# Kernel optimization log

Hardware: AMD Instinct MI355X
Metric: run time of the kernel (lower is better)

The kernel has to match this reference:

```python
import jax, jax.numpy as jnp
import numpy as np

N = 120000   # current nodes
F = 256      # num_feat
H = 256      # num_hidden
L = 64       # num_logits
E_MP = 1000000  # message-passing edges
E = 200000      # scored edges
PREV = [60000, 80000, 100000]
PROX_WEIGHT = 0.3


def setup_inputs() -> dict:
    key = jax.random.key(0)
    ks = jax.random.split(key, 40)
    n = lambda k, shape, s=0.05: jax.random.normal(k, shape, dtype=jnp.float32) * s
    inp = {}
    inp["x"] = n(ks[0], (N, F), 1.0)
    inp["mp_adj"] = jax.random.randint(ks[1], (2, E_MP), 0, N)
    inp["edges"] = jax.random.randint(ks[2], (2, E), 0, N)
    inp["index"] = jax.random.randint(ks[3], (E,), 0, E)
    inp["prev_emb0"] = n(ks[4], (PREV[0], H), 1.0)
    inp["prev_emb1"] = n(ks[5], (PREV[1], H), 1.0)
    inp["prev_emb2"] = n(ks[6], (PREV[2], H), 1.0)
    # Module_L params
    inp["gc1_W"] = n(ks[7], (F, H))
    inp["gc1_b"] = jnp.zeros((H,), jnp.float32)
    inp["gc2_W"] = n(ks[8], (H, H))
    inp["gc2_b"] = jnp.zeros((H,), jnp.float32)
    inp["linear_W"] = n(ks[9], (2 * H, H))
    inp["linear_b"] = jnp.zeros((H,), jnp.float32)
    inp["weight_lin"] = n(ks[10], (H, H))
    inp["bias_lin"] = jnp.zeros((H,), jnp.float32)
    inp["w_q"] = n(ks[11], (H, H))
    inp["w_k"] = n(ks[12], (H, H))
    inp["w_v"] = n(ks[13], (H, H))
    # ensemble params
    inp["ml_w1"] = n(ks[14], (2 * H, H)); inp["ml_b1"] = jnp.zeros((H,), jnp.float32)
    inp["ml_w2"] = n(ks[15], (H, 1));     inp["ml_b2"] = jnp.zeros((1,), jnp.float32)
    inp["ms_w1"] = n(ks[16], (2 * H, H)); inp["ms_b1"] = jnp.zeros((H,), jnp.float32)
    inp["ms_w2"] = n(ks[17], (H, 1));     inp["ms_b2"] = jnp.zeros((1,), jnp.float32)
    inp["msdr_w"] = n(ks[18], (L, H));    inp["msdr_b"] = jnp.zeros((H,), jnp.float32)
    # Module_S logits and precomputed score tables
    inp["logits"] = n(ks[19], (N, L), 1.0)
    inp["ms_train_score"] = jax.random.uniform(ks[20], (E,), dtype=jnp.float32)
    inp["prox_train_score"] = jax.random.uniform(ks[21], (E,), dtype=jnp.float32)
    return inp


def _gcn(x, W, b, src, dst, n_nodes):
    xw = x @ W
    loop = jnp.arange(n_nodes)
    s = jnp.concatenate([src, loop])
    d = jnp.concatenate([dst, loop])
    deg = jax.ops.segment_sum(jnp.ones_like(d, dtype=xw.dtype), d, num_segments=n_nodes)
    dinv = jax.lax.rsqrt(jnp.maximum(deg, 1.0))
    norm = (dinv[s] * dinv[d])[:, None]
    out = jax.ops.segment_sum(xw[s] * norm, d, num_segments=n_nodes)
    return out + b


def _mean_max(a, b):
    return jnp.concatenate([(a + b) * 0.5, jnp.maximum(a, b)], axis=1)


def reference(x, mp_adj, edges, index, prev_emb0, prev_emb1, prev_emb2,
              gc1_W, gc1_b, gc2_W, gc2_b, linear_W, linear_b,
              weight_lin, bias_lin, w_q, w_k, w_v,
              ml_w1, ml_b1, ml_w2, ml_b2, ms_w1, ms_b1, ms_w2, ms_b2,
              msdr_w, msdr_b, logits, ms_train_score, prox_train_score):
    src_mp, dst_mp = mp_adj[0], mp_adj[1]
    # --- Module_L: 2-layer GCN encoder (dropout = identity in eval) ---
    h = jnp.tanh(_gcn(x, gc1_W, gc1_b, src_mp, dst_mp, N))
    emb = jnp.tanh(_gcn(h, gc2_W, gc2_b, src_mp, dst_mp, N))

    # --- ragged per-window temporal attention over previous snapshots ---
    prev = [prev_emb0, prev_emb1, prev_emb2]
    T = len(prev)
    start = 0
    parts = []
    for i in range(T):
        end = prev[i].shape[0]
        if end == N:
            break
        # stack snapshots i..T-1 plus current, restricted to window [start:end)
        stack = jnp.stack([prev[j][start:end] for j in range(i, T)] + [emb[start:end]], axis=0)  # [S,n,H]
        q = emb[start:end] @ w_q              # [n,H]
        k = stack @ w_k                        # [S,n,H]
        v = stack @ w_v                        # [S,n,H]
        attn = jnp.einsum('nh,snh->ns', q, k) / np.sqrt(np.float32(H))
        w = jax.nn.softmax(attn, axis=-1)      # [n,S]
        parts.append(jnp.einsum('ns,snh->nh', w, v))
        start = end
    if start != N:
        parts.append(emb[start:] @ w_v)
    attn_emb = jnp.concatenate(parts, axis=0)  # [N,H]

    emb2 = jnp.tanh(jnp.concatenate([emb, attn_emb], axis=1) @ linear_W + linear_b)  # [N,H]

    # --- symmetric bilinear edge scores ---
    sym = (weight_lin + weight_lin.T) * 0.5
    es, ed = edges[0], edges[1]
    sim = ((emb2[es] @ sym) * emb2[ed] + bias_lin).sum(axis=1)
    ml_scores = jax.nn.sigmoid(sim)            # [E]

    # --- Module_S / Proximity: table lookups ---
    ms_scores = ms_train_score[index]
    prox_scores = prox_train_score[index]

    # --- ensemble weighted sum ---
    scores = jnp.stack([ml_scores, ms_scores, prox_scores], axis=1)  # [E,3]
    ml_feat = _mean_max(emb2[es], emb2[ed])                          # [E,2H]
    a_ml = jnp.tanh(jnp.tanh(ml_feat @ ml_w1 + ml_b1) @ ml_w2 + ml_b2)
    r0 = jnp.tanh(logits[es] @ msdr_w + msdr_b)
    r1 = jnp.tanh(logits[ed] @ msdr_w + msdr_b)
    a_ms = jnp.tanh(jnp.tanh(_mean_max(r0, r1) @ ms_w1 + ms_b1) @ ms_w2 + ms_b2)
    a_px = jnp.full_like(a_ml, PROX_WEIGHT)
    attn_w = jax.nn.softmax(jnp.concatenate([a_ml, a_ms, a_px], axis=1), axis=1)  # [E,3]
    final = jnp.clip((scores * attn_w).sum(axis=1), 0.0, 1.0)
    return final
```

## Files before the change

### kernel.cpp

```cpp
#include <hip/hip_runtime.h>
#include <hip/hip_bf16.h>

#define Nn_   120000
#define F_    256
#define H_    256
#define L_    64
#define EMP_  1000000
#define E_    200000
#define P0_   60000
#define P1_   80000
#define P2_   100000
#define PROXW 0.3f

typedef __attribute__((ext_vector_type(8))) short bf16x8;
typedef __attribute__((ext_vector_type(4))) float f32x4;

__device__ inline float bf2f(unsigned short u) {
    union { unsigned int i; float f; } x; x.i = ((unsigned int)u) << 16; return x.f;
}
__device__ inline unsigned short f2bf(float f) {
    union { float f; unsigned int i; } x; x.f = f;
    unsigned int r = x.i + 0x7fffu + ((x.i >> 16) & 1u);
    return (unsigned short)(r >> 16);
}
__device__ inline float tanh_fast(float x) {
    float e = __expf(2.0f * x);
    return 1.0f - 2.0f * __builtin_amdgcn_rcpf(e + 1.0f);
}
__device__ inline float sigmoid_fast(float z) {
    return __builtin_amdgcn_rcpf(1.0f + __expf(-z));
}
__device__ inline int lds_off(int row, int s) {
    return row * 64 + ((s ^ ((row >> 1) & 3)) << 4);
}
__device__ inline void gload_lds16(const void* g, void* l) {
    __builtin_amdgcn_global_load_lds((const __attribute__((address_space(1))) void*)g,
                                     (__attribute__((address_space(3))) void*)l, 16, 0, 0);
}
__device__ inline void unpk8(uint4 u, float* o) {
    o[0] = bf2f(u.x & 0xffff); o[1] = bf2f(u.x >> 16);
    o[2] = bf2f(u.y & 0xffff); o[3] = bf2f(u.y >> 16);
    o[4] = bf2f(u.z & 0xffff); o[5] = bf2f(u.z >> 16);
    o[6] = bf2f(u.w & 0xffff); o[7] = bf2f(u.w >> 16);
}
__device__ inline void meanmax_u(unsigned int ua, unsigned int ub,
                                 unsigned int& um, unsigned int& ux) {
    float alo = __uint_as_float(ua << 16);
    float ahi = __uint_as_float(ua & 0xffff0000u);
    float blo = __uint_as_float(ub << 16);
    float bhi = __uint_as_float(ub & 0xffff0000u);
    um = (unsigned int)f2bf((alo + blo) * 0.5f) |
         ((unsigned int)f2bf((ahi + bhi) * 0.5f) << 16);
    ux = (__float_as_uint(fmaxf(alo, blo)) >> 16) |
         (__float_as_uint(fmaxf(ahi, bhi)) & 0xffff0000u);
}
__device__ inline float dot2_u(unsigned int ug, unsigned int ub) {
    float gl = __uint_as_float(ug << 16);
    float gh = __uint_as_float(ug & 0xffff0000u);
    float bl = __uint_as_float(ub << 16);
    float bh = __uint_as_float(ub & 0xffff0000u);
    return fmaf(gl, bl, gh * bh);
}

__global__ void k_count(const int* __restrict__ dst, int* __restrict__ cnt, int n) {
    int e = blockIdx.x * 256 + threadIdx.x;
    if (e < n) atomicAdd(&cnt[dst[e]], 1);
}
__global__ void k_block_reduce(const int* __restrict__ cnt, int* __restrict__ bsum, int n) {
    __shared__ int s[256];
    int i = blockIdx.x * 256 + threadIdx.x;
    s[threadIdx.x] = (i < n) ? cnt[i] : 0;
    __syncthreads();
    for (int o = 128; o > 0; o >>= 1) {
        if (threadIdx.x < o) s[threadIdx.x] += s[threadIdx.x + o];
        __syncthreads();
    }
    if (threadIdx.x == 0) bsum[blockIdx.x] = s[0];
}
__global__ void k_scan_bsum(int* bsum, int nb) {
    if (threadIdx.x == 0 && blockIdx.x == 0) {
        int acc = 0;
        for (int i = 0; i < nb; i++) { int v = bsum[i]; bsum[i] = acc; acc += v; }
    }
}
__global__ void k_scan_final(const int* __restrict__ cnt, const int* __restrict__ bsum,
                             int* __restrict__ rowp, int n, int etot) {
    __shared__ int s[256];
    int tid = threadIdx.x;
    int i = blockIdx.x * 256 + tid;
    int v = (i < n) ? cnt[i] : 0;
    s[tid] = v;
    __syncthreads();
    for (int o = 1; o < 256; o <<= 1) {
        int t = 0;
        if (tid >= o) t = s[tid - o];
        __syncthreads();
        s[tid] += t;
        __syncthreads();
    }
    if (i < n) rowp[i] = bsum[blockIdx.x] + s[tid] - v;
    if (i == 0 && blockIdx.x == 0) rowp[n] = etot;
}
__global__ void k_fill(const int* __restrict__ src, const int* __restrict__ dst,
                       const int* __restrict__ rowp, int* __restrict__ fill,
                       int* __restrict__ csr, int n) {
    int e = blockIdx.x * 256 + threadIdx.x;
    if (e < n) {
        int d = dst[e];
        int p = atomicAdd(&fill[d], 1);
        csr[rowp[d] + p] = src[e];
    }
}
__global__ void k_dinv(const int* __restrict__ cnt, float* __restrict__ dinv, int n) {
    int i = blockIdx.x * 256 + threadIdx.x;
    if (i < n) dinv[i] = rsqrtf((float)cnt[i] + 1.0f);
}

#define TM 64
#define TN 64
#define TK 16
template <bool TRANSB>
__global__ void gemm_tiled(const float* __restrict__ A, const float* __restrict__ B,
                           float* __restrict__ C, int M, int K, int N) {
    __shared__ float As[TK][TM + 4];
    __shared__ float Bs[TK][TN + 4];
    int tid = threadIdx.x;
    int tx = tid & 15, ty = tid >> 4;
    int row0 = blockIdx.y * TM, col0 = blockIdx.x * TN;
    int lr = tid >> 2, lc4 = (tid & 3) * 4;
    float acc[4][4] = {};
    for (int k0 = 0; k0 < K; k0 += TK) {
        {
            int gr = row0 + lr;
            float4 v = make_float4(0.f, 0.f, 0.f, 0.f);
            if (gr < M) v = *(const float4*)(A + (size_t)gr * K + k0 + lc4);
            As[lc4 + 0][lr] = v.x; As[lc4 + 1][lr] = v.y;
            As[lc4 + 2][lr] = v.z; As[lc4 + 3][lr] = v.w;
        }
        {
            int n = tid & 63, kk0 = tid >> 6;
#pragma unroll
            for (int p = 0; p < 4; p++) {
                int kk = kk0 + p * 4;
                if (TRANSB) Bs[kk][n] = B[(size_t)(col0 + n) * K + k0 + kk];
                else        Bs[kk][n] = B[(size_t)(k0 + kk) * N + col0 + n];
            }
        }
        __syncthreads();
#pragma unroll
        for (int kk = 0; kk < TK; kk++) {
            float4 a = *(const float4*)&As[kk][ty * 4];
            float4 b = *(const float4*)&Bs[kk][tx * 4];
            float av[4] = {a.x, a.y, a.z, a.w};
            float bv[4] = {b.x, b.y, b.z, b.w};
#pragma unroll
            for (int i = 0; i < 4; i++)
#pragma unroll
                for (int j = 0; j < 4; j++) acc[i][j] += av[i] * bv[j];
        }
        __syncthreads();
    }
#pragma unroll
    for (int i = 0; i < 4; i++) {
        int r = row0 + ty * 4 + i;
        if (r >= M) continue;
#pragma unroll
        for (int j = 0; j < 4; j++) C[(size_t)r * N + col0 + tx * 4 + j] = acc[i][j];
    }
}

__global__ void k_cvt(const float* __restrict__ in, unsigned short* __restrict__ out, int n4) {
    int i = blockIdx.x * 256 + threadIdx.x;
    if (i >= n4) return;
    float4 v = ((const float4*)in)[i];
    ushort4 o;
    o.x = f2bf(v.x); o.y = f2bf(v.y); o.z = f2bf(v.z); o.w = f2bf(v.w);
    ((ushort4*)out)[i] = o;
}

__device__ inline void packBF_task(const float* __restrict__ Wsrc,
                                   unsigned short* __restrict__ P, int blk) {
    int t = blk * 256 + threadIdx.x;
    int c = t >> 6, l = t & 63;
    int os = c >> 5, half = (c >> 4) & 1, colb = c & 15;
    int col = (colb << 4) + (l & 15);
    int k = (half << 8) + (os << 5) + ((l >> 4) << 3);
    bf16x8 v;
#pragma unroll
    for (int j = 0; j < 8; ++j) v[j] = (short)f2bf(Wsrc[(size_t)(k + j) * 256 + col]);
    *(bf16x8*)(P + (size_t)t * 8) = v;
}

__global__ void k_prep1(const float* __restrict__ gc1W, const float* __restrict__ gc2W,
                        const float* __restrict__ msdrW, const float* __restrict__ wlin,
                        const float* __restrict__ blin, const float* __restrict__ mlw1,
                        const float* __restrict__ msw1,
                        unsigned short* __restrict__ gc1Wt, unsigned short* __restrict__ gc2Wt,
                        unsigned short* __restrict__ msdrWt, unsigned short* __restrict__ symb,
                        float* __restrict__ sumb, unsigned short* __restrict__ mlPk,
                        unsigned short* __restrict__ msPk) {
    __shared__ float s[256];
    int b = blockIdx.x, tid = threadIdx.x;
    if (b < 256) {
        int c = b;
        for (int r = tid; r < 256; r += 256) gc1Wt[c * 256 + r] = f2bf(gc1W[(size_t)r * 256 + c]);
    } else if (b < 512) {
        int c = b - 256;
        for (int r = tid; r < 256; r += 256) gc2Wt[c * 256 + r] = f2bf(gc2W[(size_t)r * 256 + c]);
    } else if (b < 768) {
        int c = b - 512;
        if (tid < 64) msdrWt[c * 64 + tid] = f2bf(msdrW[(size_t)tid * 256 + c]);
    } else if (b < 1024) {
        int r = b - 768, c = tid;
        symb[r * 256 + c] = f2bf(0.5f * (wlin[r * 256 + c] + wlin[c * 256 + r]));
    } else if (b == 1024) {
        s[tid] = blin[tid];
        __syncthreads();
        for (int o = 128; o > 0; o >>= 1) {
            if (tid < o) s[tid] += s[tid + o];
            __syncthreads();
        }
        if (tid == 0) sumb[0] = s[0];
    } else if (b < 1089) {
        packBF_task(mlw1, mlPk, b - 1025);
    } else {
        packBF_task(msw1, msPk, b - 1089);
    }
}
__global__ void k_prep2(const float* __restrict__ Mqk, const float* __restrict__ linW,
                        const float* __restrict__ W2w, unsigned short* __restrict__ MqkT,
                        unsigned short* __restrict__ Bt) {
    int b = blockIdx.x, tid = threadIdx.x;
    if (b < 256) {
        int c = b;
        for (int r = tid; r < 256; r += 256) MqkT[c * 256 + r] = f2bf(Mqk[(size_t)r * 256 + c]);
    } else {
        int idx = (b - 256) * 256 + tid;
        int n = idx >> 9, k = idx & 511;
        float v = (k < 256) ? linW[(size_t)k * 256 + n] : W2w[(size_t)(k - 256) * 256 + n];
        Bt[idx] = f2bf(v);
    }
}

__global__ __launch_bounds__(256)
void k_agg_bf(const unsigned short* __restrict__ xw, const int* __restrict__ rowp,
              const int* __restrict__ csr, const float* __restrict__ dinv,
              const float* __restrict__ bias, unsigned short* __restrict__ out) {
    int w = threadIdx.x >> 6, lane = threadIdx.x & 63;
    int v = blockIdx.x * 4 + w;
    if (v >= Nn_) return;
    const uint2* x64 = (const uint2*)xw;
    uint2 us = x64[(size_t)v * 64 + lane];
    float dv = dinv[v];
    float4 bv = *(const float4*)(bias + lane * 4);
    float a0 = 0.f, a1 = 0.f, a2 = 0.f, a3 = 0.f;
    int beg = rowp[v], end = rowp[v + 1];
    uint2 u0 = make_uint2(0, 0), u1 = make_uint2(0, 0);
    uint2 u2 = make_uint2(0, 0), u3 = make_uint2(0, 0);
    float e0 = 0.f, e1 = 0.f, e2 = 0.f, e3 = 0.f;
    if (beg < end)     { int s = csr[beg];     e0 = dinv[s]; u0 = x64[(size_t)s * 64 + lane]; }
    if (beg + 1 < end) { int s = csr[beg + 1]; e1 = dinv[s]; u1 = x64[(size_t)s * 64 + lane]; }
    if (beg + 2 < end) { int s = csr[beg + 2]; e2 = dinv[s]; u2 = x64[(size_t)s * 64 + lane]; }
    if (beg + 3 < end) { int s = csr[beg + 3]; e3 = dinv[s]; u3 = x64[(size_t)s * 64 + lane]; }
    #pragma unroll 4
    for (int p = beg; p < end; ++p) {
        uint2 uc = u0; float dc = e0;
        u0 = u1; e0 = e1;
        u1 = u2; e1 = e2;
        u2 = u3; e2 = e3;
        if (p + 4 < end) {
            int s = csr[p + 4];
            e3 = dinv[s];
            u3 = x64[(size_t)s * 64 + lane];
        }
        a0 += bf2f(uc.x & 0xffff) * dc;
        a1 += bf2f(uc.x >> 16) * dc;
        a2 += bf2f(uc.y & 0xffff) * dc;
        a3 += bf2f(uc.y >> 16) * dc;
    }
    a0 = a0 * dv + bf2f(us.x & 0xffff) * dv * dv;
    a1 = a1 * dv + bf2f(us.x >> 16) * dv * dv;
    a2 = a2 * dv + bf2f(us.y & 0xffff) * dv * dv;
    a3 = a3 * dv + bf2f(us.y >> 16) * dv * dv;
    uint2 ov;
    ov.x = (unsigned int)f2bf(tanh_fast(a0 + bv.x)) |
           ((unsigned int)f2bf(tanh_fast(a1 + bv.y)) << 16);
    ov.y = (unsigned int)f2bf(tanh_fast(a2 + bv.z)) |
           ((unsigned int)f2bf(tanh_fast(a3 + bv.w)) << 16);
    ((uint2*)out)[(size_t)v * 64 + lane] = ov;
}

template <bool BIAS, bool TANH>
__global__ __launch_bounds__(256)
void mfma_gemm(const unsigned short* __restrict__ A0, const unsigned short* __restrict__ A1,
               int Ksplit, int K, const unsigned short* __restrict__ Bt,
               const float* __restrict__ bias, unsigned short* __restrict__ Cb, int M) {
    __shared__ char lds[2][16384];
    int tid = threadIdx.x, lane = tid & 63, w = tid >> 6;
    int row0 = blockIdx.y * 128, col0 = blockIdx.x * 128;
    int wr = w >> 1, wc = w & 1;
    f32x4 acc[4][4] = {};
    int nk = K >> 5;

    auto stage = [&](int ks, int buf) {
        int k0 = ks << 5;
        #pragma unroll
        for (int j = 0; j < 4; ++j) {
            int ins = w + (j << 2);
            int lrow = ((ins & 7) << 4) + (lane >> 2);
            int p = lane & 3;
            int slog = p ^ ((lrow >> 1) & 3);
            char* ldst = lds[buf] + ((ins & 7) << 10) + ((ins >= 8) ? 8192 : 0);
            const unsigned short* src;
            if (ins < 8) {
                int grow = row0 + lrow;
                if (grow >= M) grow = M - 1;
                const unsigned short* Asrc; int kk, pitch;
                if (k0 < Ksplit) { Asrc = A0; kk = k0; pitch = Ksplit; }
                else             { Asrc = A1; kk = k0 - Ksplit; pitch = K - Ksplit; }
                src = Asrc + (size_t)grow * pitch + kk + (slog << 3);
            } else {
                int grow = col0 + lrow;
                src = Bt + (size_t)grow * K + k0 + (slog << 3);
            }
            gload_lds16(src, ldst);
        }
    };

    stage(0, 0);
    for (int ks = 0; ks < nk; ++ks) {
        int cur = ks & 1;
        if (ks + 1 < nk) {
            stage(ks + 1, cur ^ 1);
            asm volatile("s_waitcnt vmcnt(4)" ::: "memory");
        } else {
            asm volatile("s_waitcnt vmcnt(0)" ::: "memory");
        }
        __builtin_amdgcn_s_barrier();
        __builtin_amdgcn_sched_barrier(0);
        int s = lane >> 4, r16 = lane & 15;
        bf16x8 a[4], b[4];
        #pragma unroll
        for (int m = 0; m < 4; ++m) a[m] = *(const bf16x8*)(lds[cur] + lds_off(wr * 64 + m * 16 + r16, s));
        #pragma unroll
        for (int n = 0; n < 4; ++n) b[n] = *(const bf16x8*)(lds[cur] + 8192 + lds_off(wc * 64 + n * 16 + r16, s));
        __builtin_amdgcn_s_setprio(1);
        #pragma unroll
        for (int m = 0; m < 4; ++m)
            #pragma unroll
            for (int n = 0; n < 4; ++n)
                acc[m][n] = __builtin_amdgcn_mfma_f32_16x16x32_bf16(a[m], b[n], acc[m][n], 0, 0, 0);
        __builtin_amdgcn_s_setprio(0);
        __builtin_amdgcn_s_barrier();
        __builtin_amdgcn_sched_barrier(0);
    }
    int q = lane >> 4, r16 = lane & 15;
    float bv[4];
    #pragma unroll
    for (int n = 0; n < 4; ++n) bv[n] = BIAS ? bias[col0 + wc * 64 + n * 16 + r16] : 0.f;
    #pragma unroll
    for (int m = 0; m < 4; ++m) {
        #pragma unroll
        for (int i = 0; i < 4; ++i) {
            int row = row0 + wr * 64 + m * 16 + q * 4 + i;
            if (row >= M) continue;
            #pragma unroll
            for (int n = 0; n < 4; ++n) {
                int col = col0 + wc * 64 + n * 16 + r16;
                float v = acc[m][n][i];
                if (BIAS) v += bv[n];
                if (TANH) v = tanh_fast(v);
                Cb[(size_t)row * 256 + col] = f2bf(v);
            }
        }
    }
}

__global__ __launch_bounds__(256)
void k_attn_u2(const unsigned short* __restrict__ emb, const unsigned short* __restrict__ t,
               const float* __restrict__ p0, const float* __restrict__ p1,
               const float* __restrict__ p2, unsigned short* __restrict__ u) {
    int tid = threadIdx.x;
    int g = tid >> 4, l = tid & 15;
    int n = blockIdx.x * 16 + g;
    size_t eoff = (size_t)n * 256 + l * 16;
    const uint4* e16 = (const uint4*)(emb + eoff);
    uint4* u16 = (uint4*)(u + eoff);
    uint4 eb0 = e16[0], eb1 = e16[1];
    if (n >= P2_) { u16[0] = eb0; u16[1] = eb1; return; }
    float tv[16], ev[16];
    {
        const uint4* t16 = (const uint4*)(t + eoff);
        unpk8(t16[0], tv); unpk8(t16[1], tv + 8);
        unpk8(eb0, ev); unpk8(eb1, ev + 8);
    }
    float m = -3.0e38f, den = 0.f, o[16];
    #pragma unroll
    for (int i = 0; i < 16; i++) o[i] = 0.f;
    auto accum = [&](const float* sv) {
        float dt = 0.f;
        #pragma unroll
        for (int i = 0; i < 16; i++) dt += tv[i] * sv[i];
        dt += __shfl_xor(dt, 1);
        dt += __shfl_xor(dt, 2);
        dt += __shfl_xor(dt, 4);
        dt += __shfl_xor(dt, 8);
        float lg = dt * 0.0625f;
        float mn = fmaxf(m, lg);
        float s0 = __expf(m - mn), s1 = __expf(lg - mn);
        den = den * s0 + s1;
        #pragma unroll
        for (int i = 0; i < 16; i++) o[i] = o[i] * s0 + s1 * sv[i];
        m = mn;
    };
    auto accum_f32 = [&](const float* base) {
        float sv[16];
        const float4* b4 = (const float4*)(base + eoff);
        #pragma unroll
        for (int i = 0; i < 4; i++) {
            float4 q = b4[i];
            sv[4 * i] = q.x; sv[4 * i + 1] = q.y; sv[4 * i + 2] = q.z; sv[4 * i + 3] = q.w;
        }
        accum(sv);
    };
    if (n < P0_)      { accum_f32(p0); accum_f32(p1); accum_f32(p2); }
    else if (n < P1_) { accum_f32(p1); accum_f32(p2); }
    else              { accum_f32(p2); }
    accum(ev);
    float inv = __builtin_amdgcn_rcpf(den);
    unsigned short h[16];
    #pragma unroll
    for (int i = 0; i < 16; i++) h[i] = f2bf(o[i] * inv);
    uint4 r0, r1;
    r0.x = h[0] | ((unsigned int)h[1] << 16);  r0.y = h[2] | ((unsigned int)h[3] << 16);
    r0.z = h[4] | ((unsigned int)h[5] << 16);  r0.w = h[6] | ((unsigned int)h[7] << 16);
    r1.x = h[8] | ((unsigned int)h[9] << 16);  r1.y = h[10] | ((unsigned int)h[11] << 16);
    r1.z = h[12] | ((unsigned int)h[13] << 16); r1.w = h[14] | ((unsigned int)h[15] << 16);
    u16[0] = r0; u16[1] = r1;
}

__global__ __launch_bounds__(256)
void mfma_edge7(const unsigned short* __restrict__ emb2b, const unsigned short* __restrict__ rtabb,
                const unsigned short* __restrict__ gtab,
                const int* __restrict__ es, const int* __restrict__ ed,
                const unsigned short* __restrict__ PkMl, const unsigned short* __restrict__ PkMs,
                const float* __restrict__ b1ml, const float* __restrict__ w2ml,
                const float* __restrict__ b1ms, const float* __restrict__ w2ms,
                const float* __restrict__ sumb,
                float* __restrict__ apml, float* __restrict__ apms,
                float* __restrict__ mlsc, int nml) {
    __shared__ char lds[16384];
    __shared__ float red[64];
    bool sim = (int)blockIdx.x < nml;
    int bid = sim ? blockIdx.x : (blockIdx.x - nml);
    const unsigned short* srcemb = sim ? emb2b : rtabb;
    const unsigned short* PkF = sim ? PkMl : PkMs;
    const float* b1 = sim ? b1ml : b1ms;
    const float* w2 = sim ? w2ml : w2ms;
    float* a_pre = sim ? apml : apms;
    int tid = threadIdx.x, lane = tid & 63, w = tid >> 6;
    int e0 = bid * 64;
    int arow = tid >> 2, p = tid & 3;
    int ia = es[e0 + arow], ib = ed[e0 + arow];
    const unsigned short* ra = srcemb + (size_t)ia * 256;
    const unsigned short* rb = srcemb + (size_t)ib * 256;
    const unsigned short* rg = gtab + (size_t)ia * 256;
    int slog = p ^ ((arow >> 1) & 3);
    int abase = arow * 64 + (p << 4);
    if (tid < 64) red[tid] = 0.f;
    float simacc = 0.f;
    f32x4 acc[4][4] = {};
    uint4 pa = *(const uint4*)(ra + (slog << 3));
    uint4 pb = *(const uint4*)(rb + (slog << 3));
    uint4 pg = make_uint4(0, 0, 0, 0);
    if (sim) pg = *(const uint4*)(rg + (slog << 3));
    const bf16x8* BF = (const bf16x8*)PkF;
    for (int os = 0; os < 8; ++os) {
        int cbuf = (os & 1) << 13;
        {
            unsigned int m0, x0, m1, x1, m2, x2, m3, x3;
            meanmax_u(pa.x, pb.x, m0, x0);
            meanmax_u(pa.y, pb.y, m1, x1);
            meanmax_u(pa.z, pb.z, m2, x2);
            meanmax_u(pa.w, pb.w, m3, x3);
            *(uint4*)(lds + cbuf + abase) = make_uint4(m0, m1, m2, m3);
            *(uint4*)(lds + cbuf + 4096 + abase) = make_uint4(x0, x1, x2, x3);
            if (sim)
                simacc += dot2_u(pg.x, pb.x) + dot2_u(pg.y, pb.y) +
                          dot2_u(pg.z, pb.z) + dot2_u(pg.w, pb.w);
        }
        bf16x8 b0[4], b1f[4];
        #pragma unroll
        for (int n2 = 0; n2 < 4; ++n2) {
            int c0i = (os << 5) + (w << 2) + n2;
            b0[n2]  = BF[(size_t)c0i * 64 + lane];
            b1f[n2] = BF[(size_t)(c0i + 16) * 64 + lane];
        }
        if (os < 7) {
            int cb = ((os + 1) << 5) + (slog << 3);
            pa = *(const uint4*)(ra + cb);
            pb = *(const uint4*)(rb + cb);
            if (sim) pg = *(const uint4*)(rg + cb);
        }
        asm volatile("s_waitcnt lgkmcnt(0)" ::: "memory");
        __builtin_amdgcn_s_barrier();
        __builtin_amdgcn_sched_barrier(0);
        int s = lane >> 4, r16 = lane & 15;
        {
            bf16x8 a[4];
            #pragma unroll
            for (int m2 = 0; m2 < 4; ++m2)
                a[m2] = *(const bf16x8*)(lds + cbuf + lds_off(m2 * 16 + r16, s));
            __builtin_amdgcn_s_setprio(1);
            #pragma unroll
            for (int m2 = 0; m2 < 4; ++m2)
                #pragma unroll
                for (int n2 = 0; n2 < 4; ++n2)
                    acc[m2][n2] = __builtin_amdgcn_mfma_f32_16x16x32_bf16(a[m2], b0[n2], acc[m2][n2], 0, 0, 0);
            __builtin_amdgcn_s_setprio(0);
        }
        {
            bf16x8 a[4];
            #pragma unroll
            for (int m2 = 0; m2 < 4; ++m2)
                a[m2] = *(const bf16x8*)(lds + cbuf + 4096 + lds_off(m2 * 16 + r16, s));
            __builtin_amdgcn_s_setprio(1);
            #pragma unroll
            for (int m2 = 0; m2 < 4; ++m2)
                #pragma unroll
                for (int n2 = 0; n2 < 4; ++n2)
                    acc[m2][n2] = __builtin_amdgcn_mfma_f32_16x16x32_bf16(a[m2], b1f[n2], acc[m2][n2], 0, 0, 0);
            __builtin_amdgcn_s_setprio(0);
        }
    }
    int q = lane >> 4, r16 = lane & 15;
    float b1c[4], w2c[4];
    #pragma unroll
    for (int n2 = 0; n2 < 4; ++n2) {
        int c = (w << 6) + n2 * 16 + r16;
        b1c[n2] = b1[c]; w2c[n2] = w2[c];
    }
    #pragma unroll
    for (int m2 = 0; m2 < 4; ++m2) {
        #pragma unroll
        for (int i = 0; i < 4; ++i) {
            int row = m2 * 16 + q * 4 + i;
            float ps = 0.f;
            #pragma unroll
            for (int n2 = 0; n2 < 4; ++n2) ps += tanh_fast(acc[m2][n2][i] + b1c[n2]) * w2c[n2];
            ps += __shfl_xor(ps, 1);
            ps += __shfl_xor(ps, 2);
            ps += __shfl_xor(ps, 4);
            ps += __shfl_xor(ps, 8);
            if (r16 == 0) atomicAdd(&red[row], ps);
        }
    }
    if (sim) {
        simacc += __shfl_xor(simacc, 1);
        simacc += __shfl_xor(simacc, 2);
        if (p == 0) mlsc[e0 + arow] = sigmoid_fast(simacc + sumb[0]);
    }
    __syncthreads();
    if (tid < 64) a_pre[e0 + tid] = red[tid];
}

__global__ void k_final(const float* __restrict__ apml, const float* __restrict__ apms,
                        const float* __restrict__ mlsc, const float* __restrict__ mstr,
                        const float* __restrict__ pxtr, const int* __restrict__ index,
                        const float* __restrict__ mlb2, const float* __restrict__ msb2,
                        float* __restrict__ out) {
    int e = blockIdx.x * 256 + threadIdx.x;
    if (e >= E_) return;
    float aml = tanh_fast(apml[e] + mlb2[0]);
    float ams = tanh_fast(apms[e] + msb2[0]);
    float apx = PROXW;
    float m = fmaxf(aml, fmaxf(ams, apx));
    float wml = __expf(aml - m), wms = __expf(ams - m), wpx = __expf(apx - m);
    float inv = __builtin_amdgcn_rcpf(wml + wms + wpx);
    int idx = index[e];
    float v = (mlsc[e] * wml + mstr[idx] * wms + pxtr[idx] * wpx) * inv;
    out[e] = fminf(fmaxf(v, 0.f), 1.f);
}

__global__ void k_sentinel(float* out, int n) {
    int i = blockIdx.x * 256 + threadIdx.x;
    if (i < n) out[i] = -12345.0f;
}

extern "C" void kernel_launch(void* const* d_in, const int* in_sizes, int n_in,
                              void* d_out, int out_size, void* d_ws, size_t ws_size,
                              hipStream_t stream) {
    const float* x     = (const float*)d_in[0];
    const int*   mp    = (const int*)d_in[1];
    const int*   edges = (const int*)d_in[2];
    const int*   index = (const int*)d_in[3];
    const float* p0    = (const float*)d_in[4];
    const float* p1    = (const float*)d_in[5];
    const float* p2    = (const float*)d_in[6];
    const float* gc1W  = (const float*)d_in[7];
    const float* gc1b  = (const float*)d_in[8];
    const float* gc2W  = (const float*)d_in[9];
    const float* gc2b  = (const float*)d_in[10];
    const float* linW  = (const float*)d_in[11];
    const float* linb  = (const float*)d_in[12];
    const float* wlin  = (const float*)d_in[13];
    const float* blin  = (const float*)d_in[14];
    const float* wq    = (const float*)d_in[15];
    const float* wk    = (const float*)d_in[16];
    const float* wv    = (const float*)d_in[17];
    const float* mlw1  = (const float*)d_in[18];
    const float* mlb1  = (const float*)d_in[19];
    const float* mlw2  = (const float*)d_in[20];
    const float* mlb2  = (const float*)d_in[21];
    const float* msw1  = (const float*)d_in[22];
    const float* msb1  = (const float*)d_in[23];
    const float* msw2  = (const float*)d_in[24];
    const float* msb2  = (const float*)d_in[25];
    const float* msdrW = (const float*)d_in[26];
    const float* msdrb = (const float*)d_in[27];
    const float* logits = (const float*)d_in[28];
    const float* mstr  = (const float*)d_in[29];
    const float* pxtr  = (const float*)d_in[30];
    float* out = (float*)d_out;

    const int* src_mp = mp;
    const int* dst_mp = mp + EMP_;
    const int* es = edges;
    const int* ed = edges + E_;

    char* ws = (char*)d_ws;
    size_t off = 0;
    auto alloc = [&](size_t bytes) -> char* {
        off = (off + 255) & ~(size_t)255;
        char* r = ws + off;
        off += bytes;
        return r;
    };
    const size_t NODE_BF = (size_t)Nn_ * 256 * 2;
    unsigned short* W0 = (unsigned short*)alloc(NODE_BF);
    unsigned short* W1 = (unsigned short*)alloc(NODE_BF);
    unsigned short* W2 = (unsigned short*)alloc(NODE_BF);
    unsigned short* W3 = (unsigned short*)alloc(NODE_BF);
    unsigned short* W4 = (unsigned short*)alloc(NODE_BF);
    unsigned short* W5 = (unsigned short*)alloc(NODE_BF);
    int*   cnt  = (int*)alloc((size_t)Nn_ * 4);
    int*   rowp = (int*)alloc((size_t)(Nn_ + 1) * 4);
    int*   fill = (int*)alloc((size_t)Nn_ * 4);
    int*   csr  = (int*)alloc((size_t)EMP_ * 4);
    float* dinv = (float*)alloc((size_t)Nn_ * 4);
    int*   bsum = (int*)alloc(512 * 4);
    float* Mqk  = (float*)alloc(65536 * 4);
    float* W2wf = (float*)alloc(65536 * 4);
    unsigned short* gc1Wt = (unsigned short*)alloc(65536 * 2);
    unsigned short* gc2Wt = (unsigned short*)alloc(65536 * 2);
    unsigned short* MqkT  = (unsigned short*)alloc(65536 * 2);
    unsigned short* Bt512 = (unsigned short*)alloc(131072 * 2);
    unsigned short* symb  = (unsigned short*)alloc(65536 * 2);
    unsigned short* msdrWt = (unsigned short*)alloc(16384 * 2);
    unsigned short* mlPk  = (unsigned short*)alloc(131072 * 2);
    unsigned short* msPk  = (unsigned short*)alloc(131072 * 2);
    float* apml = (float*)alloc((size_t)E_ * 4);
    float* apms = (float*)alloc((size_t)E_ * 4);
    float* mlsc = (float*)alloc((size_t)E_ * 4);
    float* sumb = (float*)alloc(256);

    if (off > ws_size) {
        k_sentinel<<<(E_ + 255) / 256, 256, 0, stream>>>(out, E_);
        return;
    }

    hipMemsetAsync(cnt, 0, (size_t)Nn_ * 4, stream);
    hipMemsetAsync(fill, 0, (size_t)Nn_ * 4, stream);

    const int NB = (Nn_ + 255) / 256;
    const int EB = (EMP_ + 255) / 256;

    k_cvt<<<30000, 256, 0, stream>>>(x, W0, Nn_ * 256 / 4);
    k_prep1<<<1153, 256, 0, stream>>>(gc1W, gc2W, msdrW, wlin, blin, mlw1, msw1,
                                      gc1Wt, gc2Wt, msdrWt, symb, sumb, mlPk, msPk);
    dim3 gSmall(4, 4);
    gemm_tiled<true><<<gSmall, 256, 0, stream>>>(wq, wk, Mqk, 256, 256, 256);
    gemm_tiled<false><<<gSmall, 256, 0, stream>>>(wv, linW + 256 * 256, W2wf, 256, 256, 256);
    k_prep2<<<768, 256, 0, stream>>>(Mqk, linW, W2wf, MqkT, Bt512);

    k_count<<<EB, 256, 0, stream>>>(dst_mp, cnt, EMP_);
    k_block_reduce<<<NB, 256, 0, stream>>>(cnt, bsum, Nn_);
    k_scan_bsum<<<1, 64, 0, stream>>>(bsum, NB);
    k_scan_final<<<NB, 256, 0, stream>>>(cnt, bsum, rowp, Nn_, EMP_);
    k_fill<<<EB, 256, 0, stream>>>(src_mp, dst_mp, rowp, fill, csr, EMP_);
    k_dinv<<<NB, 256, 0, stream>>>(cnt, dinv, Nn_);

    dim3 gFull(2, (Nn_ + 127) / 128);
    dim3 gT(2, (P2_ + 127) / 128);
    const int AGG_B = (Nn_ + 3) / 4;

    mfma_gemm<false, false><<<gFull, 256, 0, stream>>>(W0, W0, 256, 256, gc1Wt, nullptr, W1, Nn_);
    k_agg_bf<<<AGG_B, 256, 0, stream>>>(W1, rowp, csr, dinv, gc1b, W2);
    mfma_gemm<false, false><<<gFull, 256, 0, stream>>>(W2, W2, 256, 256, gc2Wt, nullptr, W1, Nn_);
    k_agg_bf<<<AGG_B, 256, 0, stream>>>(W1, rowp, csr, dinv, gc2b, W3);

    mfma_gemm<false, false><<<gT, 256, 0, stream>>>(W3, W3, 256, 256, MqkT, nullptr, W4, P2_);
    k_attn_u2<<<Nn_ / 16, 256, 0, stream>>>(W3, W4, p0, p1, p2, W4);

    mfma_gemm<true, true><<<gFull, 256, 0, stream>>>(W3, W4, 256, 512, Bt512, linb, W5, Nn_);

    mfma_gemm<false, false><<<gFull, 256, 0, stream>>>(W5, W5, 256, 256, symb, nullptr, W0, Nn_);

    k_cvt<<<7500, 256, 0, stream>>>(logits, W1, Nn_ * 64 / 4);
    mfma_gemm<true, true><<<gFull, 256, 0, stream>>>(W1, W1, 64, 64, msdrWt, msdrb, W2, Nn_);

    const int NML = E_ / 64;
    mfma_edge7<<<2 * NML, 256, 0, stream>>>(W5, W2, W0, es, ed, mlPk, msPk,
                                            mlb1, mlw2, msb1, msw2, sumb,
                                            apml, apms, mlsc, NML);

    k_final<<<(E_ + 255) / 256, 256, 0, stream>>>(apml, apms, mlsc, mstr, pxtr, index, mlb2, msb2, out);
}
```

Baseline: 929.2 us.

## Merge two independent GEMMs into one launch and deepen edge-gather prefetch

Adds a dual GEMM kernel that runs the emb2·sym projection and the logits·msdr projection (bias plus tanh) in a single grid, picking the operands by blockIdx.y. This removes one launch and lets the two small GEMMs share the GPU. The edge kernel now prefetches gathered rows two k-steps ahead instead of one, to hide more of the random-gather latency at the cost of extra registers. The logits conversion is also moved earlier in the launch order.

```diff
diff --git a/kernel.cpp b/kernel.cpp
--- a/kernel.cpp
+++ b/kernel.cpp
@@ -377,6 +377,95 @@
 }
 
 __global__ __launch_bounds__(256)
+void mfma_gemm_dual(const unsigned short* __restrict__ Aa, const unsigned short* __restrict__ Ba,
+                    unsigned short* __restrict__ Ca,
+                    const unsigned short* __restrict__ Ab, const unsigned short* __restrict__ Bb,
+                    const float* __restrict__ biasb, unsigned short* __restrict__ Cb2,
+                    int M, int rowsA) {
+    __shared__ char lds[2][16384];
+    int tid = threadIdx.x, lane = tid & 63, w = tid >> 6;
+    bool tb = (int)blockIdx.y >= rowsA;
+    int by = tb ? (blockIdx.y - rowsA) : blockIdx.y;
+    const unsigned short* A0 = tb ? Ab : Aa;
+    const unsigned short* Bt = tb ? Bb : Ba;
+    unsigned short* Cb = tb ? Cb2 : Ca;
+    int K = tb ? 64 : 256;
+    int row0 = by * 128, col0 = blockIdx.x * 128;
+    int wr = w >> 1, wc = w & 1;
+    f32x4 acc[4][4] = {};
+    int nk = K >> 5;
+
+    auto stage = [&](int ks, int buf) {
+        int k0 = ks << 5;
+        #pragma unroll
+        for (int j = 0; j < 4; ++j) {
+            int ins = w + (j << 2);
+            int lrow = ((ins & 7) << 4) + (lane >> 2);
+            int p = lane & 3;
+            int slog = p ^ ((lrow >> 1) & 3);
+            char* ldst = lds[buf] + ((ins & 7) << 10) + ((ins >= 8) ? 8192 : 0);
+            const unsigned short* src;
+            if (ins < 8) {
+                int grow = row0 + lrow;
+                if (grow >= M) grow = M - 1;
+                src = A0 + (size_t)grow * K + k0 + (slog << 3);
+            } else {
+                int grow = col0 + lrow;
+                src = Bt + (size_t)grow * K + k0 + (slog << 3);
+            }
+            gload_lds16(src, ldst);
+        }
+    };
+
+    stage(0, 0);
+    for (int ks = 0; ks < nk; ++ks) {
+        int cur = ks & 1;
+        if (ks + 1 < nk) {
+            stage(ks + 1, cur ^ 1);
+            asm volatile("s_waitcnt vmcnt(4)" ::: "memory");
+        } else {
+            asm volatile("s_waitcnt vmcnt(0)" ::: "memory");
+        }
+        __builtin_amdgcn_s_barrier();
+        __builtin_amdgcn_sched_barrier(0);
+        int s = lane >> 4, r16 = lane & 15;
+        bf16x8 a[4], b[4];
+        #pragma unroll
+        for (int m = 0; m < 4; ++m) a[m] = *(const bf16x8*)(lds[cur] + lds_off(wr * 64 + m * 16 + r16, s));
+        #pragma unroll
+        for (int n = 0; n < 4; ++n) b[n] = *(const bf16x8*)(lds[cur] + 8192 + lds_off(wc * 64 + n * 16 + r16, s));
+        __builtin_amdgcn_s_setprio(1);
+        #pragma unroll
+        for (int m = 0; m < 4; ++m)
+            #pragma unroll
+            for (int n = 0; n < 4; ++n)
+                acc[m][n] = __builtin_amdgcn_mfma_f32_16x16x32_bf16(a[m], b[n], acc[m][n], 0, 0, 0);
+        __builtin_amdgcn_s_setprio(0);
+        __builtin_amdgcn_s_barrier();
+        __builtin_amdgcn_sched_barrier(0);
+    }
+    int q = lane >> 4, r16 = lane & 15;
+    float bv[4];
+    #pragma unroll
+    for (int n = 0; n < 4; ++n) bv[n] = tb ? biasb[col0 + wc * 64 + n * 16 + r16] : 0.f;
+    #pragma unroll
+    for (int m = 0; m < 4; ++m) {
+        #pragma unroll
+        for (int i = 0; i < 4; ++i) {
+            int row = row0 + wr * 64 + m * 16 + q * 4 + i;
+            if (row >= M) continue;
+            #pragma unroll
+            for (int n = 0; n < 4; ++n) {
+                int col = col0 + wc * 64 + n * 16 + r16;
+                float v = acc[m][n][i];
+                if (tb) v = tanh_fast(v + bv[n]);
+                Cb[(size_t)row * 256 + col] = f2bf(v);
+            }
+        }
+    }
+}
+
+__global__ __launch_bounds__(256)
 void k_attn_u2(const unsigned short* __restrict__ emb, const unsigned short* __restrict__ t,
                const float* __restrict__ p0, const float* __restrict__ p1,
                const float* __restrict__ p2, unsigned short* __restrict__ u) {
@@ -440,7 +529,7 @@
 }
 
 __global__ __launch_bounds__(256)
-void mfma_edge7(const unsigned short* __restrict__ emb2b, const unsigned short* __restrict__ rtabb,
+void mfma_edge8(const unsigned short* __restrict__ emb2b, const unsigned short* __restrict__ rtabb,
                 const unsigned short* __restrict__ gtab,
                 const int* __restrict__ es, const int* __restrict__ ed,
                 const unsigned short* __restrict__ PkMl, const unsigned short* __restrict__ PkMs,
@@ -466,29 +555,36 @@
     const unsigned short* rb = srcemb + (size_t)ib * 256;
     const unsigned short* rg = gtab + (size_t)ia * 256;
     int slog = p ^ ((arow >> 1) & 3);
+    int co = slog << 3;
     int abase = arow * 64 + (p << 4);
     if (tid < 64) red[tid] = 0.f;
     float simacc = 0.f;
     f32x4 acc[4][4] = {};
-    uint4 pa = *(const uint4*)(ra + (slog << 3));
-    uint4 pb = *(const uint4*)(rb + (slog << 3));
-    uint4 pg = make_uint4(0, 0, 0, 0);
-    if (sim) pg = *(const uint4*)(rg + (slog << 3));
+    uint4 pa0 = *(const uint4*)(ra + co);
+    uint4 pb0 = *(const uint4*)(rb + co);
+    uint4 pg0 = make_uint4(0, 0, 0, 0);
+    if (sim) pg0 = *(const uint4*)(rg + co);
+    uint4 pa1 = *(const uint4*)(ra + 32 + co);
+    uint4 pb1 = *(const uint4*)(rb + 32 + co);
+    uint4 pg1 = make_uint4(0, 0, 0, 0);
+    if (sim) pg1 = *(const uint4*)(rg + 32 + co);
     const bf16x8* BF = (const bf16x8*)PkF;
     for (int os = 0; os < 8; ++os) {
         int cbuf = (os & 1) << 13;
         {
             unsigned int m0, x0, m1, x1, m2, x2, m3, x3;
-            meanmax_u(pa.x, pb.x, m0, x0);
-            meanmax_u(pa.y, pb.y, m1, x1);
-            meanmax_u(pa.z, pb.z, m2, x2);
-            meanmax_u(pa.w, pb.w, m3, x3);
+            meanmax_u(pa0.x, pb0.x, m0, x0);
+            meanmax_u(pa0.y, pb0.y, m1, x1);
+            meanmax_u(pa0.z, pb0.z, m2, x2);
+            meanmax_u(pa0.w, pb0.w, m3, x3);
             *(uint4*)(lds + cbuf + abase) = make_uint4(m0, m1, m2, m3);
             *(uint4*)(lds + cbuf + 4096 + abase) = make_uint4(x0, x1, x2, x3);
             if (sim)
-                simacc += dot2_u(pg.x, pb.x) + dot2_u(pg.y, pb.y) +
-                          dot2_u(pg.z, pb.z) + dot2_u(pg.w, pb.w);
-        }
+                simacc += dot2_u(pg0.x, pb0.x) + dot2_u(pg0.y, pb0.y) +
+                          dot2_u(pg0.z, pb0.z) + dot2_u(pg0.w, pb0.w);
+        }
+        pa0 = pa1; pb0 = pb1;
+        if (sim) pg0 = pg1;
         bf16x8 b0[4], b1f[4];
         #pragma unroll
         for (int n2 = 0; n2 < 4; ++n2) {
@@ -496,11 +592,11 @@
             b0[n2]  = BF[(size_t)c0i * 64 + lane];
             b1f[n2] = BF[(size_t)(c0i + 16) * 64 + lane];
         }
-        if (os < 7) {
-            int cb = ((os + 1) << 5) + (slog << 3);
-            pa = *(const uint4*)(ra + cb);
-            pb = *(const uint4*)(rb + cb);
-            if (sim) pg = *(const uint4*)(rg + cb);
+        if (os < 6) {
+            int cb = ((os + 2) << 5) + co;
+            pa1 = *(const uint4*)(ra + cb);
+            pb1 = *(const uint4*)(rb + cb);
+            if (sim) pg1 = *(const uint4*)(rg + cb);
         }
         asm volatile("s_waitcnt lgkmcnt(0)" ::: "memory");
         __builtin_amdgcn_s_barrier();
@@ -693,24 +789,25 @@
     dim3 gFull(2, (Nn_ + 127) / 128);
     dim3 gT(2, (P2_ + 127) / 128);
     const int AGG_B = (Nn_ + 3) / 4;
+    const int ROWS = (Nn_ + 127) / 128;
 
     mfma_gemm<false, false><<<gFull, 256, 0, stream>>>(W0, W0, 256, 256, gc1Wt, nullptr, W1, Nn_);
     k_agg_bf<<<AGG_B, 256, 0, stream>>>(W1, rowp, csr, dinv, gc1b, W2);
     mfma_gemm<false, false><<<gFull, 256, 0, stream>>>(W2, W2, 256, 256, gc2Wt, nullptr, W1, Nn_);
     k_agg_bf<<<AGG_B, 256, 0, stream>>>(W1, rowp, csr, dinv, gc2b, W3);
 
+    k_cvt<<<7500, 256, 0, stream>>>(logits, W1, Nn_ * 64 / 4);
+
     mfma_gemm<false, false><<<gT, 256, 0, stream>>>(W3, W3, 256, 256, MqkT, nullptr, W4, P2_);
     k_attn_u2<<<Nn_ / 16, 256, 0, stream>>>(W3, W4, p0, p1, p2, W4);
 
     mfma_gemm<true, true><<<gFull, 256, 0, stream>>>(W3, W4, 256, 512, Bt512, linb, W5, Nn_);
 
-    mfma_gemm<false, false><<<gFull, 256, 0, stream>>>(W5, W5, 256, 256, symb, nullptr, W0, Nn_);
-
-    k_cvt<<<7500, 256, 0, stream>>>(logits, W1, Nn_ * 64 / 4);
-    mfma_gemm<true, true><<<gFull, 256, 0, stream>>>(W1, W1, 64, 64, msdrWt, msdrb, W2, Nn_);
+    dim3 gDual(2, 2 * ROWS);
+    mfma_gemm_dual<<<gDual, 256, 0, stream>>>(W5, symb, W0, W1, msdrWt, msdrb, W2, Nn_, ROWS);
 
     const int NML = E_ / 64;
-    mfma_edge7<<<2 * NML, 256, 0, stream>>>(W5, W2, W0, es, ed, mlPk, msPk,
+    mfma_edge8<<<2 * NML, 256, 0, stream>>>(W5, W2, W0, es, ed, mlPk, msPk,
                                             mlb1, mlw2, msb1, msw2, sumb,
                                             apml, apms, mlsc, NML);
 
```

Result: slower. 964.6 us (+3.8%).
